# Optimization experiments

Measured on AMD Instinct MI355X. Metric: run time of the kernel, lower is better.

Reference implementation:

```python
import jax, jax.numpy as jnp
import numpy as np


def _conv2d(x, w, b, stride):
    y = jax.lax.conv_general_dilated(x, w, (stride, stride), [(1, 1), (1, 1)],
                                     dimension_numbers=('NCHW', 'OIHW', 'NCHW'))
    return y + b[None, :, None, None]


def _bn(x, g, b, m, v, eps=1e-5):
    scale = g * jax.lax.rsqrt(v + eps)
    return x * scale[None, :, None, None] + (b - m * scale)[None, :, None, None]


def _ln(x, g, b, eps=1e-5):
    mu = x.mean(-1, keepdims=True)
    var = x.var(-1, keepdims=True)
    return (x - mu) * jax.lax.rsqrt(var + eps) * g + b


def _sru_layer(x, W, v, b, lng, lnb):
    # x: (T,B,D); W: (2,D,4d); v,b: (2,2,d). Bidirectional SRU layer with
    # layer-norm on input, tanh activation, k=4 (highway transform of input).
    xn = _ln(x, lng, lnb)
    d = W.shape[-1] // 4
    B = x.shape[1]
    outs = []
    for direc in range(2):
        xi = xn if direc == 0 else xn[::-1]
        U = xi @ W[direc]                       # (T,B,4d)
        xt, fp, rp, xp = jnp.split(U, 4, axis=-1)
        vf, vr = v[direc, 0], v[direc, 1]
        bf, br = b[direc, 0], b[direc, 1]

        def step(c, u):
            xt_, fp_, rp_, xp_ = u
            f = jax.nn.sigmoid(fp_ + vf * c + bf)   # forget gate, peeks c_{t-1}
            r = jax.nn.sigmoid(rp_ + vr * c + br)   # reset/highway gate
            c_new = f * c + (1.0 - f) * xt_
            h = r * jnp.tanh(c_new) + (1.0 - r) * xp_
            return c_new, h

        c0 = jnp.zeros((B, d), x.dtype)
        _, h = jax.lax.scan(step, c0, (xt, fp, rp, xp))
        outs.append(h if direc == 0 else h[::-1])
    return jnp.concatenate(outs, axis=-1)       # (T,B,2d)


def _forward(x, cnn_w, cnn_b, res_c1w, res_c1b, res_bn1g, res_bn1b, res_bn1m,
             res_bn1v, res_c2w, res_c2b, res_bn2g, res_bn2b, res_bn2m, res_bn2v,
             proj_W, sru_W, sru_v, sru_b, sru_lng, sru_lnb,
             cls_lng, cls_lnb, cls_W1, cls_W2):
    y = _conv2d(x, cnn_w, cnn_b, 2)              # (B,32,F/2,T/2)
    for i in range(res_c1w.shape[0]):            # residual CNN blocks
        r = y
        y = jax.nn.relu(_bn(_conv2d(y, res_c1w[i], res_c1b[i], 1),
                            res_bn1g[i], res_bn1b[i], res_bn1m[i], res_bn1v[i]))
        y = _bn(_conv2d(y, res_c2w[i], res_c2b[i], 1),
                res_bn2g[i], res_bn2b[i], res_bn2m[i], res_bn2v[i])
        y = jax.nn.relu(y + r)
    B, C, H, T = y.shape
    y = y.reshape(B, C * H, T).transpose(2, 0, 1)   # (T,B,C*H)
    y = y @ proj_W                                   # proj_input_to_hidden_first
    for l in range(sru_W.shape[0]):
        y = _sru_layer(y, sru_W[l], sru_v[l], sru_b[l], sru_lng[l], sru_lnb[l])
    y = y.transpose(1, 0, 2)                         # (B,T,2*hid)
    y = _ln(y, cls_lng, cls_lnb)
    y = jax.nn.relu(y @ cls_W1)
    return y @ cls_W2                                # (B,T,n_vocab+1)


def setup_inputs() -> dict:
    key = jax.random.key(0)
    ks = iter(jax.random.split(key, 40))
    nk = lambda: next(ks)
    B, T, F, C = 16, 1024, 128, 32
    L_cnn, L_rnn, hid, vocab = 3, 4, 512, 28
    Din = (F // 2) * C          # 2048
    D = 2 * hid                 # 1024 (bidirectional width)
    rnd = lambda shape, s=0.02: jax.random.normal(nk(), shape, jnp.float32) * s
    return {
        'x': jax.random.normal(nk(), (B, 1, F, T), jnp.float32),
        'cnn_w': rnd((C, 1, 3, 3), 0.1), 'cnn_b': jnp.zeros((C,), jnp.float32),
        'res_c1w': rnd((L_cnn, C, C, 3, 3), 0.05), 'res_c1b': jnp.zeros((L_cnn, C), jnp.float32),
        'res_bn1g': jnp.ones((L_cnn, C), jnp.float32), 'res_bn1b': jnp.zeros((L_cnn, C), jnp.float32),
        'res_bn1m': jnp.zeros((L_cnn, C), jnp.float32), 'res_bn1v': jnp.ones((L_cnn, C), jnp.float32),
        'res_c2w': rnd((L_cnn, C, C, 3, 3), 0.05), 'res_c2b': jnp.zeros((L_cnn, C), jnp.float32),
        'res_bn2g': jnp.ones((L_cnn, C), jnp.float32), 'res_bn2b': jnp.zeros((L_cnn, C), jnp.float32),
        'res_bn2m': jnp.zeros((L_cnn, C), jnp.float32), 'res_bn2v': jnp.ones((L_cnn, C), jnp.float32),
        'proj_W': rnd((Din, D)),
        'sru_W': rnd((L_rnn, 2, D, 4 * hid)),
        'sru_v': rnd((L_rnn, 2, 2, hid)),
        'sru_b': jnp.zeros((L_rnn, 2, 2, hid), jnp.float32),
        'sru_lng': jnp.ones((L_rnn, D), jnp.float32), 'sru_lnb': jnp.zeros((L_rnn, D), jnp.float32),
        'cls_lng': jnp.ones((D,), jnp.float32), 'cls_lnb': jnp.zeros((D,), jnp.float32),
        'cls_W1': rnd((D, hid)), 'cls_W2': rnd((hid, vocab + 1)),
    }


def reference(x, cnn_w, cnn_b, res_c1w, res_c1b, res_bn1g, res_bn1b, res_bn1m,
              res_bn1v, res_c2w, res_c2b, res_bn2g, res_bn2b, res_bn2m, res_bn2v,
              proj_W, sru_W, sru_v, sru_b, sru_lng, sru_lnb,
              cls_lng, cls_lnb, cls_W1, cls_W2):
    return _forward(x, cnn_w, cnn_b, res_c1w, res_c1b, res_bn1g, res_bn1b,
                    res_bn1m, res_bn1v, res_c2w, res_c2b, res_bn2g, res_bn2b,
                    res_bn2m, res_bn2v, proj_W, sru_W, sru_v, sru_b,
                    sru_lng, sru_lnb, cls_lng, cls_lnb, cls_W1, cls_W2)
```

## Files before the change

kernel.cpp:

```cpp
#include <hip/hip_runtime.h>
#include <cstddef>

#define DEVFN __device__ __forceinline__

typedef __attribute__((ext_vector_type(8))) short short8;
typedef __attribute__((ext_vector_type(8))) unsigned short ushort8;
typedef __attribute__((ext_vector_type(4))) float f32x4;
typedef __attribute__((ext_vector_type(2))) unsigned int u32x2;

DEVFN float sigmoidf_(float x) { return 1.0f / (1.0f + __expf(-x)); }
DEVFN float tanh_fast(float x) {
    float e = __expf(2.0f * x);
    return 1.0f - 2.0f / (e + 1.0f);
}
DEVFN unsigned short f2bf(float f) {
    unsigned int u = __float_as_uint(f);
    return (unsigned short)((u + 0x7FFFu + ((u >> 16) & 1u)) >> 16);
}
DEVFN float b2f(unsigned int bits) { return __uint_as_float(bits << 16); }

DEVFN void gload_lds16(const ushort* g, ushort* l) {
    __builtin_amdgcn_global_load_lds(
        (const __attribute__((address_space(1))) unsigned int*)g,
        (__attribute__((address_space(3))) unsigned int*)l, 16, 0, 0);
}

#define PADN 17371008u

__global__ __launch_bounds__(256)
void ring_zero(ushort* A, ushort* B)
{
    int idx = blockIdx.x * 256 + threadIdx.x;
    if (idx >= 296960) return;
    size_t uoff;
    if (idx < 263168) {
        int b = idx / 16448, r = idx % 16448;
        int hs = (r < 8224) ? 0 : 65;
        int o = (r < 8224) ? r : r - 8224;
        uoff = (((size_t)(b * 66 + hs) * 514) * 32 + (size_t)o * 2) >> 1;
    } else {
        int j = idx - 263168;
        int b = j / 2112, r = j % 2112;
        int hs = r >> 5, e = r & 31;
        int wsp = (e < 16) ? 0 : 513;
        int c2 = e & 15;
        uoff = (((size_t)(b * 66 + hs) * 514 + wsp) * 32 + (size_t)c2 * 2) >> 1;
    }
    ((uint*)A)[uoff] = 0; ((uint*)B)[uoff] = 0;
}

__global__ __launch_bounds__(256)
void conv_wprep(const float* __restrict__ c1w, const float* __restrict__ c2w,
                ushort* __restrict__ whi, ushort* __restrict__ wlo)
{
    const int lay = blockIdx.x;
    const int i = lay >> 1;
    const float* src = (lay & 1) ? (c2w + i * 9216) : (c1w + i * 9216);
    for (int e = threadIdx.x; e < 9216; e += 256) {
        int co = e / 288, rem = e % 288, ci = rem / 9, q = rem % 9;
        float v = src[e];
        unsigned short hi = f2bf(v);
        unsigned short lo = f2bf(v - b2f(hi));
        int dst = ((lay * 9 + q) * 32 + co) * 32 + ci;
        whi[dst] = hi; wlo[dst] = lo;
    }
}

__global__ __launch_bounds__(256)
void conv_stem_p(const float* __restrict__ x, const float* __restrict__ w,
                 const float* __restrict__ cb, ushort* __restrict__ Xhi)
{
    const int b = blockIdx.z;
    const int h = blockIdx.y * 4 + (threadIdx.x >> 6);
    const int wc = blockIdx.x * 64 + (threadIdx.x & 63);
    float iv[9];
#pragma unroll
    for (int kh = 0; kh < 3; ++kh)
#pragma unroll
        for (int kw = 0; kw < 3; ++kw) {
            int ih = 2 * h - 1 + kh, iw = 2 * wc - 1 + kw;
            iv[kh * 3 + kw] = (ih >= 0 && ih < 128 && iw >= 0 && iw < 1024)
                ? x[(size_t)b * 131072 + (size_t)ih * 1024 + iw] : 0.0f;
        }
    unsigned short hi[32];
#pragma unroll
    for (int co = 0; co < 32; ++co) {
        const float* wp = w + co * 9;
        float a = cb[co];
#pragma unroll
        for (int q = 0; q < 9; ++q) a = fmaf(iv[q], wp[q], a);
        hi[co] = f2bf(a);
    }
    const size_t o = ((size_t)(b * 66 + h + 1) * 514 + wc + 1) * 32;
#pragma unroll
    for (int v = 0; v < 4; ++v) {
        ushort8 uh;
#pragma unroll
        for (int e = 0; e < 8; ++e) uh[e] = hi[v * 8 + e];
        *(ushort8*)(Xhi + o + v * 8) = uh;
    }
}

template <int RES>
__global__ __launch_bounds__(256)
void conv_mfma(const ushort* __restrict__ Phi,
               const ushort* __restrict__ gwhi, const ushort* __restrict__ gwlo,
               const float* __restrict__ g, const float* __restrict__ bbn,
               const float* __restrict__ mn, const float* __restrict__ vn,
               const float* __restrict__ cbv,
               const ushort* __restrict__ Rhi, ushort* __restrict__ Ohi)
{
    __shared__ __align__(16) ushort Wsh[9216], Wsl[9216];
    const int tid = threadIdx.x, lane = tid & 63, wv = tid >> 6;
    const int b = blockIdx.z, h0 = blockIdx.y * 4, w0 = blockIdx.x * 128;

    for (int i = tid; i < 1152; i += 256) {
        ((uint4*)Wsh)[i] = ((const uint4*)gwhi)[i];
        ((uint4*)Wsl)[i] = ((const uint4*)gwlo)[i];
    }
    __syncthreads();

    const int wr = wv * 32;
    const int fr = lane & 15, fk = (lane >> 4) * 8;
    const int lo0 = (wr + fr) * 32 + fk;
    const int lo1 = (wr + 16 + fr) * 32 + fk;

    float sc[2], sh[2];
#pragma unroll
    for (int n = 0; n < 2; ++n) {
        const int co = n * 16 + fr;
        sc[n] = g[co] * rsqrtf(vn[co] + 1e-5f);
        sh[n] = bbn[co] - mn[co] * sc[n] + cbv[co] * sc[n];
    }

    short8 A[3][2][3];
#define LOADROW(SL, PR)                                                        \
    {                                                                          \
        const size_t rb_ = ((size_t)(b * 66 + (PR)) * 514 + w0) * 32;          \
        _Pragma("unroll")                                                      \
        for (int kw_ = 0; kw_ < 3; ++kw_) {                                    \
            A[SL][0][kw_] = *(const short8*)(Phi + rb_ + kw_ * 32 + lo0);      \
            A[SL][1][kw_] = *(const short8*)(Phi + rb_ + kw_ * 32 + lo1);      \
        }                                                                      \
    }

    LOADROW(0, h0);
    LOADROW(1, h0 + 1);

#pragma unroll
    for (int hh = 0; hh < 4; ++hh) {
        LOADROW((hh + 2) % 3, h0 + hh + 2);
        f32x4 acc[2][2];
#pragma unroll
        for (int m = 0; m < 2; ++m)
#pragma unroll
            for (int n = 0; n < 2; ++n) acc[m][n] = (f32x4){0.f, 0.f, 0.f, 0.f};
#pragma unroll
        for (int kh = 0; kh < 3; ++kh) {
            const int sl = (hh + kh) % 3;
#pragma unroll
            for (int kw = 0; kw < 3; ++kw) {
                const int q = kh * 3 + kw;
                short8 ah0 = A[sl][0][kw];
                short8 ah1 = A[sl][1][kw];
                short8 bh0 = *(const short8*)&Wsh[q * 1024 + fr * 32 + fk];
                short8 bh1 = *(const short8*)&Wsh[q * 1024 + (16 + fr) * 32 + fk];
                short8 bl0 = *(const short8*)&Wsl[q * 1024 + fr * 32 + fk];
                short8 bl1 = *(const short8*)&Wsl[q * 1024 + (16 + fr) * 32 + fk];
                acc[0][0] = __builtin_amdgcn_mfma_f32_16x16x32_bf16(ah0, bh0, acc[0][0], 0, 0, 0);
                acc[0][1] = __builtin_amdgcn_mfma_f32_16x16x32_bf16(ah0, bh1, acc[0][1], 0, 0, 0);
                acc[1][0] = __builtin_amdgcn_mfma_f32_16x16x32_bf16(ah1, bh0, acc[1][0], 0, 0, 0);
                acc[1][1] = __builtin_amdgcn_mfma_f32_16x16x32_bf16(ah1, bh1, acc[1][1], 0, 0, 0);
                acc[0][0] = __builtin_amdgcn_mfma_f32_16x16x32_bf16(ah0, bl0, acc[0][0], 0, 0, 0);
                acc[0][1] = __builtin_amdgcn_mfma_f32_16x16x32_bf16(ah0, bl1, acc[0][1], 0, 0, 0);
                acc[1][0] = __builtin_amdgcn_mfma_f32_16x16x32_bf16(ah1, bl0, acc[1][0], 0, 0, 0);
                acc[1][1] = __builtin_amdgcn_mfma_f32_16x16x32_bf16(ah1, bl1, acc[1][1], 0, 0, 0);
            }
        }
#pragma unroll
        for (int m = 0; m < 2; ++m)
#pragma unroll
            for (int r = 0; r < 4; ++r) {
                const int wl = wr + m * 16 + (lane >> 4) * 4 + r;
                const size_t oidx =
                    ((size_t)(b * 66 + h0 + hh + 1) * 514 + w0 + wl + 1) * 32;
#pragma unroll
                for (int n = 0; n < 2; ++n) {
                    const int co = n * 16 + fr;
                    float val = acc[m][n][r] * sc[n] + sh[n];
                    if (RES) val += b2f(Rhi[oidx + co]);
                    val = fmaxf(val, 0.0f);
                    Ohi[oidx + co] = f2bf(val);
                }
            }
    }
#undef LOADROW
}

__global__ __launch_bounds__(256)
void gather_pad(const ushort* __restrict__ Xhi, ushort* __restrict__ xrow)
{
    __shared__ ushort tile[64 * 16 * 32];
    const int b = blockIdx.y, w0 = blockIdx.x * 16;
    for (int k = threadIdx.x; k < 4096; k += 256) {
        int h = k >> 6, rem = k & 63, wl = rem >> 2, c8 = (rem & 3) * 8;
        const ushort* src = Xhi + ((size_t)(b * 66 + h + 1) * 514 + w0 + 1 + wl) * 32 + c8;
        *(ushort8*)&tile[(h * 16 + wl) * 32 + c8] = *(const ushort8*)src;
    }
    __syncthreads();
    for (int k = threadIdx.x; k < 4096; k += 256) {
        int wl = k >> 8, rem = k & 255, c = rem >> 3, h8 = (rem & 7) * 8;
        ushort8 v;
#pragma unroll
        for (int e = 0; e < 8; ++e) v[e] = tile[((h8 + e) * 16 + wl) * 32 + c];
        *(ushort8*)&xrow[((size_t)(w0 + wl) * 16 + b) * 2048 + c * 64 + h8] = v;
    }
}

__global__ __launch_bounds__(256)
void wconv_t(const float* __restrict__ W, ushort* __restrict__ Bt,
             int K, int N, int perm, size_t wstr, size_t btstr)
{
    __shared__ float tile[64][65];
    const float* Wp = W + (size_t)blockIdx.z * wstr;
    ushort* Btp = Bt + (size_t)blockIdx.z * btstr;
    const int k0 = blockIdx.x * 64;
    const int n0 = blockIdx.y * 64;
#pragma unroll
    for (int p = 0; p < 16; ++p) {
        int idx = p * 256 + threadIdx.x;
        int kl = idx >> 6, nl = idx & 63;
        tile[kl][nl] = Wp[(size_t)(k0 + kl) * N + n0 + nl];
    }
    __syncthreads();
#pragma unroll
    for (int p = 0; p < 16; ++p) {
        int idx = p * 256 + threadIdx.x;
        int nl = idx >> 6, kl = idx & 63;
        int n = n0 + nl;
        int row = perm ? ((n & 511) * 4 + (n >> 9)) : n;
        Btp[(size_t)row * K + k0 + kl] = f2bf(tile[kl][nl]);
    }
}

__global__ __launch_bounds__(256)
void layernorm1024_bf(const float* __restrict__ x, const float* __restrict__ g,
                      const float* __restrict__ b, ushort* __restrict__ y)
{
    const size_t row = blockIdx.x;
    const float4 v = ((const float4*)(x + row * 1024))[threadIdx.x];
    float s = v.x + v.y + v.z + v.w;
    float s2 = v.x * v.x + v.y * v.y + v.z * v.z + v.w * v.w;
#pragma unroll
    for (int off = 32; off; off >>= 1) {
        s += __shfl_down(s, off);
        s2 += __shfl_down(s2, off);
    }
    __shared__ float red[2][4];
    int wid = threadIdx.x >> 6, lane = threadIdx.x & 63;
    if (lane == 0) { red[0][wid] = s; red[1][wid] = s2; }
    __syncthreads();
    s = red[0][0] + red[0][1] + red[0][2] + red[0][3];
    s2 = red[1][0] + red[1][1] + red[1][2] + red[1][3];
    float mu = s * (1.0f / 1024.0f);
    float var = s2 * (1.0f / 1024.0f) - mu * mu;
    float rstd = rsqrtf(var + 1e-5f);
    float4 gv = ((const float4*)g)[threadIdx.x];
    float4 bv = ((const float4*)b)[threadIdx.x];
    ushort4 o;
    o.x = f2bf((v.x - mu) * rstd * gv.x + bv.x);
    o.y = f2bf((v.y - mu) * rstd * gv.y + bv.y);
    o.z = f2bf((v.z - mu) * rstd * gv.z + bv.z);
    o.w = f2bf((v.w - mu) * rstd * gv.w + bv.w);
    ((ushort4*)(y + row * 1024))[threadIdx.x] = o;
}

__global__ __launch_bounds__(512, 2)
void gemm256_bf16(const ushort* __restrict__ A, const ushort* __restrict__ Bt,
                  ushort* __restrict__ C, int M, int N, int K)
{
    __shared__ __align__(16) ushort LDS[65536];
    const int tid = threadIdx.x;
    const int lane = tid & 63, w = tid >> 6;
    const int wm = w >> 2, wn = w & 3;
    const int m0 = blockIdx.y * 256, n0 = blockIdx.x * 256;
    const int fr = lane & 15, fk = (lane >> 4) * 8;
    const int NT = K >> 6;

    const int sprow = tid >> 3;
    const int scb0 = (tid & 7) * 16;
    const int wq = w * 512;

    f32x4 acc[8][4];
#pragma unroll
    for (int i = 0; i < 8; ++i)
#pragma unroll
        for (int j = 0; j < 4; ++j) acc[i][j] = (f32x4){0.f, 0.f, 0.f, 0.f};

    auto stage = [&](int dbuf, int isB, int qi, int kt) {
        const int prow = qi * 64 + sprow;
        const int sc = scb0 ^ (((prow >> 2) & 1) << 5);
        const ushort* g = (isB ? (Bt + (size_t)(n0 + prow) * K)
                               : (A + (size_t)(m0 + prow) * K))
                          + (kt << 6) + (sc >> 1);
        gload_lds16(g, LDS + (isB ? 32768 : 0) + dbuf * 16384 + qi * 4096 + wq);
    };
    auto rdA = [&](int dbuf, int mi8, int ks) -> short8 {
        const int row = wm * 128 + mi8 * 16 + fr;
        int e = (row * 64 + ks * 32 + fk) ^ (((row >> 2) & 1) << 4);
        return *(const short8*)&LDS[dbuf * 16384 + e];
    };
    auto rdB = [&](int dbuf, int ni, int ks) -> short8 {
        const int row = wn * 64 + ni * 16 + fr;
        int e = (row * 64 + ks * 32 + fk) ^ (((row >> 2) & 1) << 4);
        return *(const short8*)&LDS[32768 + dbuf * 16384 + e];
    };

#pragma unroll
    for (int qi = 0; qi < 4; ++qi) stage(0, 0, qi, 0);
#pragma unroll
    for (int qi = 0; qi < 4; ++qi) stage(0, 1, qi, 0);

    for (int kt = 0; kt < NT; ++kt) {
        const int cur = kt & 1, nxt = cur ^ 1;
        const bool more = (kt + 1 < NT);
        short8 bfr[4], afr[4];

        if (more) {
            stage(nxt, 0, 0, kt + 1); stage(nxt, 0, 1, kt + 1);
            asm volatile("s_waitcnt vmcnt(2)" ::: "memory");
        } else {
            asm volatile("s_waitcnt vmcnt(0)" ::: "memory");
        }
        __builtin_amdgcn_s_barrier();
#pragma unroll
        for (int ni = 0; ni < 4; ++ni) bfr[ni] = rdB(cur, ni, 0);
#pragma unroll
        for (int mi = 0; mi < 4; ++mi) afr[mi] = rdA(cur, mi, 0);
        __builtin_amdgcn_s_setprio(1);
#pragma unroll
        for (int mi = 0; mi < 4; ++mi)
#pragma unroll
            for (int ni = 0; ni < 4; ++ni)
                acc[mi][ni] = __builtin_amdgcn_mfma_f32_16x16x32_bf16(
                    afr[mi], bfr[ni], acc[mi][ni], 0, 0, 0);
        __builtin_amdgcn_s_setprio(0);

        if (more) { stage(nxt, 0, 2, kt + 1); stage(nxt, 0, 3, kt + 1); }
#pragma unroll
        for (int mi = 0; mi < 4; ++mi) afr[mi] = rdA(cur, 4 + mi, 0);
        __builtin_amdgcn_s_setprio(1);
#pragma unroll
        for (int mi = 0; mi < 4; ++mi)
#pragma unroll
            for (int ni = 0; ni < 4; ++ni)
                acc[4 + mi][ni] = __builtin_amdgcn_mfma_f32_16x16x32_bf16(
                    afr[mi], bfr[ni], acc[4 + mi][ni], 0, 0, 0);
        __builtin_amdgcn_s_setprio(0);

        if (more) { stage(nxt, 1, 0, kt + 1); stage(nxt, 1, 1, kt + 1); }
#pragma unroll
        for (int ni = 0; ni < 4; ++ni) bfr[ni] = rdB(cur, ni, 1);
#pragma unroll
        for (int mi = 0; mi < 4; ++mi) afr[mi] = rdA(cur, mi, 1);
        __builtin_amdgcn_s_setprio(1);
#pragma unroll
        for (int mi = 0; mi < 4; ++mi)
#pragma unroll
            for (int ni = 0; ni < 4; ++ni)
                acc[mi][ni] = __builtin_amdgcn_mfma_f32_16x16x32_bf16(
                    afr[mi], bfr[ni], acc[mi][ni], 0, 0, 0);
        __builtin_amdgcn_s_setprio(0);

        if (more) { stage(nxt, 1, 2, kt + 1); stage(nxt, 1, 3, kt + 1); }
#pragma unroll
        for (int mi = 0; mi < 4; ++mi) afr[mi] = rdA(cur, 4 + mi, 1);
        __builtin_amdgcn_s_setprio(1);
#pragma unroll
        for (int mi = 0; mi < 4; ++mi)
#pragma unroll
            for (int ni = 0; ni < 4; ++ni)
                acc[4 + mi][ni] = __builtin_amdgcn_mfma_f32_16x16x32_bf16(
                    afr[mi], bfr[ni], acc[4 + mi][ni], 0, 0, 0);
        __builtin_amdgcn_s_setprio(0);

        __builtin_amdgcn_s_barrier();
    }

#pragma unroll
    for (int mi8 = 0; mi8 < 8; ++mi8)
#pragma unroll
        for (int r = 0; r < 4; ++r) {
            const int row = wm * 128 + mi8 * 16 + (lane >> 4) * 4 + r;
#pragma unroll
            for (int ni = 0; ni < 4; ++ni)
                LDS[row * 256 + wn * 64 + ni * 16 + fr] = f2bf(acc[mi8][ni][r]);
        }
    __builtin_amdgcn_s_barrier();
    const int frow = tid >> 5, fcb = (tid & 31) * 8;
#pragma unroll
    for (int it = 0; it < 16; ++it) {
        const int row = it * 16 + frow;
        ushort8 vv = *(const ushort8*)&LDS[row * 256 + fcb];
        *(ushort8*)&C[(size_t)(m0 + row) * N + n0 + fcb] = vv;
    }
}

template <int RELU>
__global__ __launch_bounds__(256)
void gemm_bf16(const ushort* __restrict__ A, const ushort* __restrict__ Bt,
               float* __restrict__ C, int M, int N, int K)
{
    __shared__ __align__(16) ushort Sh[4][4096];
    const int tid = threadIdx.x;
    const int lane = tid & 63, w = tid >> 6;
    const int m0 = blockIdx.y * 128, n0 = blockIdx.x * 128;
    const int srow = lane >> 2;
    const int skel = (lane & 3) * 8;
    const int wr = (w >> 1) * 64, wcol = (w & 1) * 64;
    const int fr = lane & 15, fk = (lane >> 4) * 8;

    f32x4 acc[4][4];
#pragma unroll
    for (int m = 0; m < 4; ++m)
#pragma unroll
        for (int n = 0; n < 4; ++n) acc[m][n] = (f32x4){0.f, 0.f, 0.f, 0.f};

#pragma unroll
    for (int q = 0; q < 2; ++q) {
        const int ch = w * 2 + q;
        gload_lds16(A + (size_t)(m0 + ch * 16 + srow) * K + skel, &Sh[0][ch * 512]);
        gload_lds16(Bt + (size_t)(n0 + ch * 16 + srow) * K + skel, &Sh[2][ch * 512]);
    }
    __syncthreads();

    int cur = 0;
    for (int k0 = 0; k0 < K; k0 += 32) {
        if (k0 + 32 < K) {
#pragma unroll
            for (int q = 0; q < 2; ++q) {
                const int ch = w * 2 + q;
                gload_lds16(A + (size_t)(m0 + ch * 16 + srow) * K + k0 + 32 + skel,
                            &Sh[cur ^ 1][ch * 512]);
                gload_lds16(Bt + (size_t)(n0 + ch * 16 + srow) * K + k0 + 32 + skel,
                            &Sh[2 + (cur ^ 1)][ch * 512]);
            }
        }
        short8 a[4], b[4];
#pragma unroll
        for (int m = 0; m < 4; ++m)
            a[m] = *(const short8*)&Sh[cur][(wr + m * 16 + fr) * 32 + fk];
#pragma unroll
        for (int n = 0; n < 4; ++n)
            b[n] = *(const short8*)&Sh[2 + cur][(wcol + n * 16 + fr) * 32 + fk];
#pragma unroll
        for (int m = 0; m < 4; ++m)
#pragma unroll
            for (int n = 0; n < 4; ++n)
                acc[m][n] = __builtin_amdgcn_mfma_f32_16x16x32_bf16(
                    a[m], b[n], acc[m][n], 0, 0, 0);
        __syncthreads();
        cur ^= 1;
    }
#pragma unroll
    for (int m = 0; m < 4; ++m) {
#pragma unroll
        for (int r = 0; r < 4; ++r) {
            const int row = m0 + wr + m * 16 + (lane >> 4) * 4 + r;
            const size_t rb = (size_t)row * N;
#pragma unroll
            for (int n = 0; n < 4; ++n) {
                float val = acc[m][n][r];
                if (RELU) val = fmaxf(val, 0.0f);
                C[rb + n0 + wcol + n * 16 + fr] = val;
            }
        }
    }
}

__global__ __launch_bounds__(64)
void sru_scan2(const ushort* __restrict__ U, const float* __restrict__ v,
               const float* __restrict__ bb, float* __restrict__ out)
{
    const int gidx = blockIdx.x * 64 + threadIdx.x;
    const int dir = gidx >> 13;
    const int idx = gidx & 8191;
    const int j = idx & 511, b = idx >> 9;
    float vf = v[dir * 1024 + j],   vr = v[dir * 1024 + 512 + j];
    float bf_ = bb[dir * 1024 + j], br_ = bb[dir * 1024 + 512 + j];
    const size_t cb = (size_t)dir * 2048 + j * 4;
    const int co = dir * 512 + j;

    asm volatile("" : "+v"(vf), "+v"(vr), "+v"(bf_), "+v"(br_));
    asm volatile("s_waitcnt vmcnt(0)" ::: "memory");

#define TT(q_) (dir ? (511 - (q_)) : (q_))
    float c = 0.0f;
    u32x2 A[16], B[16];

#define ISSUE(dst, s_)                                                         \
    asm volatile("global_load_dwordx2 %0, %1, off"                             \
                 : "=v"(dst)                                                   \
                 : "v"(U + (((size_t)(TT(s_) * 16 + b)) << 12) + cb)           \
                 : "memory")
#define FILL(BUF, wn_)                                                         \
    {                                                                          \
        _Pragma("unroll")                                                      \
        for (int q_ = 0; q_ < 16; ++q_) ISSUE(BUF[q_], (wn_) * 16 + q_);       \
    }
#define WAITBUF(BUF)                                                           \
    asm volatile("s_waitcnt vmcnt(16)"                                         \
                 : "+v"(BUF[0]), "+v"(BUF[1]), "+v"(BUF[2]), "+v"(BUF[3]),     \
                   "+v"(BUF[4]), "+v"(BUF[5]), "+v"(BUF[6]), "+v"(BUF[7]),     \
                   "+v"(BUF[8]), "+v"(BUF[9]), "+v"(BUF[10]), "+v"(BUF[11]),   \
                   "+v"(BUF[12]), "+v"(BUF[13]), "+v"(BUF[14]), "+v"(BUF[15])  \
                 :: "memory")
#define STEP(val, s_)                                                          \
    {                                                                          \
        const int t_ = TT(s_);                                                 \
        float xt = b2f(val[0] & 0xffffu);                                      \
        float fp = b2f(val[0] >> 16);                                          \
        float rp = b2f(val[1] & 0xffffu);                                      \
        float xp = b2f(val[1] >> 16);                                          \
        float f = sigmoidf_(fp + vf * c + bf_);                                \
        float r = sigmoidf_(rp + vr * c + br_);                                \
        c = fmaf(f, c - xt, xt);                                               \
        float h = fmaf(r, tanh_fast(c) - xp, xp);                              \
        asm volatile("global_store_dword %0, %1, off"                          \
                     :: "v"(out + (((size_t)(t_ * 16 + b)) << 10) + co),       \
                        "v"(h)                                                 \
                     : "memory");                                              \
    }

    FILL(A, 0);
    for (int p = 0; p < 16; ++p) {
        const int s0 = p * 32;
        FILL(B, 2 * p + 1);
        WAITBUF(A);
#pragma unroll
        for (int q = 0; q < 16; ++q) STEP(A[q], s0 + q);
        if (p < 15) FILL(A, 2 * p + 2);
        WAITBUF(B);
#pragma unroll
        for (int q = 0; q < 16; ++q) STEP(B[q], s0 + 16 + q);
    }
#undef STEP
#undef WAITBUF
#undef FILL
#undef ISSUE
#undef TT
}

__global__ __launch_bounds__(256)
void cls_out(const float* __restrict__ h1, const float* __restrict__ W2,
             float* __restrict__ out)
{
    const int gidx = blockIdx.x * 256 + threadIdx.x;
    const int n = gidx & 31, m = gidx >> 5;
    if (n >= 29) return;
    const float4* hr = (const float4*)(h1 + (size_t)m * 512);
    float acc = 0.0f;
    for (int k4 = 0; k4 < 128; ++k4) {
        float4 hv = hr[k4];
        const float* wp = W2 + (size_t)(k4 * 4) * 29 + n;
        acc = fmaf(hv.x, wp[0],  acc);
        acc = fmaf(hv.y, wp[29], acc);
        acc = fmaf(hv.z, wp[58], acc);
        acc = fmaf(hv.w, wp[87], acc);
    }
    const int t = m >> 4, b = m & 15;
    out[((size_t)b * 512 + t) * 29 + n] = acc;
}

extern "C" void kernel_launch(void* const* d_in, const int* in_sizes, int n_in,
                              void* d_out, int out_size, void* d_ws, size_t ws_size,
                              hipStream_t stream)
{
    (void)in_sizes; (void)n_in; (void)out_size; (void)ws_size;
    const float* x      = (const float*)d_in[0];
    const float* cnn_w  = (const float*)d_in[1];
    const float* cnn_b  = (const float*)d_in[2];
    const float* c1w    = (const float*)d_in[3];
    const float* c1b    = (const float*)d_in[4];
    const float* bn1g   = (const float*)d_in[5];
    const float* bn1b   = (const float*)d_in[6];
    const float* bn1m   = (const float*)d_in[7];
    const float* bn1v   = (const float*)d_in[8];
    const float* c2w    = (const float*)d_in[9];
    const float* c2b    = (const float*)d_in[10];
    const float* bn2g   = (const float*)d_in[11];
    const float* bn2b   = (const float*)d_in[12];
    const float* bn2m   = (const float*)d_in[13];
    const float* bn2v   = (const float*)d_in[14];
    const float* projW  = (const float*)d_in[15];
    const float* sruW   = (const float*)d_in[16];
    const float* sruV   = (const float*)d_in[17];
    const float* sruB   = (const float*)d_in[18];
    const float* sruLNg = (const float*)d_in[19];
    const float* sruLNb = (const float*)d_in[20];
    const float* clsLNg = (const float*)d_in[21];
    const float* clsLNb = (const float*)d_in[22];
    const float* W1     = (const float*)d_in[23];
    const float* W2     = (const float*)d_in[24];
    float* out = (float*)d_out;
    float* ws  = (float*)d_ws;

    ushort* Xhi = (ushort*)ws;
    ushort* Thi = Xhi + PADN;
    ushort* convw_hi = (ushort*)(ws + 34742016);
    ushort* convw_lo = convw_hi + 55296;
    ushort* xrow_bf  = (ushort*)(ws + 34865152);
    ushort* xn_bf    = (ushort*)(ws + 43253760);
    ushort* Ubuf     = (ushort*)ws;
    float*  xch      = ws + 16777216;
    ushort* proj_bt  = (ushort*)(ws + 25165824);
    ushort* sru_bt   = (ushort*)(ws + 26214400);
    ushort* w1t      = (ushort*)(ws + 34603008);
    float*  h1       = ws;

    dim3 blk(256);

    ring_zero<<<1160, blk, 0, stream>>>(Xhi, Thi);
    conv_wprep<<<6, blk, 0, stream>>>(c1w, c2w, convw_hi, convw_lo);
    conv_stem_p<<<dim3(8, 16, 16), blk, 0, stream>>>(x, cnn_w, cnn_b, Xhi);
    for (int i = 0; i < 3; ++i) {
        const int l1 = 2 * i, l2 = 2 * i + 1;
        conv_mfma<0><<<dim3(4, 16, 16), blk, 0, stream>>>(
            Xhi, convw_hi + l1 * 9216, convw_lo + l1 * 9216,
            bn1g + i * 32, bn1b + i * 32, bn1m + i * 32, bn1v + i * 32,
            c1b + i * 32, nullptr, Thi);
        conv_mfma<1><<<dim3(4, 16, 16), blk, 0, stream>>>(
            Thi, convw_hi + l2 * 9216, convw_lo + l2 * 9216,
            bn2g + i * 32, bn2b + i * 32, bn2m + i * 32, bn2v + i * 32,
            c2b + i * 32, Xhi, Xhi);
    }

    wconv_t<<<dim3(32, 16, 1), blk, 0, stream>>>(projW, proj_bt, 2048, 1024, 0, 0, 0);
    wconv_t<<<dim3(16, 32, 8), blk, 0, stream>>>(sruW, sru_bt, 1024, 2048, 1,
                                                 2097152, 2097152);
    wconv_t<<<dim3(16, 8, 1), blk, 0, stream>>>(W1, w1t, 1024, 512, 0, 0, 0);

    gather_pad<<<dim3(32, 16), blk, 0, stream>>>(Xhi, xrow_bf);

    gemm_bf16<0><<<dim3(8, 64), blk, 0, stream>>>(
        xrow_bf, proj_bt, xch, 8192, 1024, 2048);

    for (int l = 0; l < 4; ++l) {
        layernorm1024_bf<<<8192, blk, 0, stream>>>(
            xch, sruLNg + l * 1024, sruLNb + l * 1024, xn_bf);
        gemm256_bf16<<<dim3(16, 32), dim3(512), 0, stream>>>(
            xn_bf, sru_bt + (size_t)l * 4194304, Ubuf, 8192, 4096, 1024);
        sru_scan2<<<256, dim3(64), 0, stream>>>(
            Ubuf, sruV + l * 2048, sruB + l * 2048, xch);
    }

    layernorm1024_bf<<<8192, blk, 0, stream>>>(xch, clsLNg, clsLNb, xn_bf);
    gemm_bf16<1><<<dim3(4, 64), blk, 0, stream>>>(
        xn_bf, w1t, h1, 8192, 512, 1024);
    cls_out<<<1024, blk, 0, stream>>>(h1, W2, out);
}
```

Measured before the change: 936.1 us.

## Split SRU scan: serial c-chain only, move highway output into fused LN kernel

```diff
diff --git a/kernel.cpp b/kernel.cpp
--- a/kernel.cpp
+++ b/kernel.cpp
@@ -6,7 +6,6 @@
 typedef __attribute__((ext_vector_type(8))) short short8;
 typedef __attribute__((ext_vector_type(8))) unsigned short ushort8;
 typedef __attribute__((ext_vector_type(4))) float f32x4;
-typedef __attribute__((ext_vector_type(2))) unsigned int u32x2;
 
 DEVFN float sigmoidf_(float x) { return 1.0f / (1.0f + __expf(-x)); }
 DEVFN float tanh_fast(float x) {
@@ -275,9 +274,64 @@
     ((ushort4*)(y + row * 1024))[threadIdx.x] = o;
 }
 
+__global__ __launch_bounds__(256)
+void lnh(const float* __restrict__ cbuf, const ushort* __restrict__ Uo,
+         const float* __restrict__ v, const float* __restrict__ bb,
+         const float* __restrict__ g, const float* __restrict__ be,
+         ushort* __restrict__ y)
+{
+    const int r = blockIdx.x, t = r >> 4;
+    const int tid = threadIdx.x, dir = tid >> 7;
+    const int jj = (tid * 4) & 511;
+    float4 cc = *(const float4*)(cbuf + (size_t)r * 1024 + tid * 4);
+    const int pr = dir ? (t == 511 ? -1 : r + 16) : (t == 0 ? -1 : r - 16);
+    float4 cp = {0.f, 0.f, 0.f, 0.f};
+    if (pr >= 0) cp = *(const float4*)(cbuf + (size_t)pr * 1024 + tid * 4);
+    ushort8 u = *(const ushort8*)(Uo + (size_t)r * 2048 + dir * 1024 + jj * 2);
+    float4 vr = *(const float4*)(v + dir * 1024 + 512 + jj);
+    float4 br = *(const float4*)(bb + dir * 1024 + 512 + jj);
+    float h[4];
+    const float cpe[4] = {cp.x, cp.y, cp.z, cp.w};
+    const float cce[4] = {cc.x, cc.y, cc.z, cc.w};
+    const float vre[4] = {vr.x, vr.y, vr.z, vr.w};
+    const float bre[4] = {br.x, br.y, br.z, br.w};
+#pragma unroll
+    for (int e = 0; e < 4; ++e) {
+        float rp = b2f(u[2 * e]);
+        float xp = b2f(u[2 * e + 1]);
+        float rg = sigmoidf_(rp + vre[e] * cpe[e] + bre[e]);
+        h[e] = fmaf(rg, tanh_fast(cce[e]) - xp, xp);
+    }
+    float s = h[0] + h[1] + h[2] + h[3];
+    float s2 = h[0] * h[0] + h[1] * h[1] + h[2] * h[2] + h[3] * h[3];
+#pragma unroll
+    for (int off = 32; off; off >>= 1) {
+        s += __shfl_down(s, off);
+        s2 += __shfl_down(s2, off);
+    }
+    __shared__ float red[2][4];
+    int wid = tid >> 6, lane = tid & 63;
+    if (lane == 0) { red[0][wid] = s; red[1][wid] = s2; }
+    __syncthreads();
+    s = red[0][0] + red[0][1] + red[0][2] + red[0][3];
+    s2 = red[1][0] + red[1][1] + red[1][2] + red[1][3];
+    float mu = s * (1.0f / 1024.0f);
+    float var = s2 * (1.0f / 1024.0f) - mu * mu;
+    float rstd = rsqrtf(var + 1e-5f);
+    float4 gv = ((const float4*)g)[tid];
+    float4 bv = ((const float4*)be)[tid];
+    ushort4 o;
+    o.x = f2bf((h[0] - mu) * rstd * gv.x + bv.x);
+    o.y = f2bf((h[1] - mu) * rstd * gv.y + bv.y);
+    o.z = f2bf((h[2] - mu) * rstd * gv.z + bv.z);
+    o.w = f2bf((h[3] - mu) * rstd * gv.w + bv.w);
+    ((ushort4*)(y + (size_t)r * 1024))[tid] = o;
+}
+
 __global__ __launch_bounds__(512, 2)
 void gemm256_bf16(const ushort* __restrict__ A, const ushort* __restrict__ Bt,
-                  ushort* __restrict__ C, int M, int N, int K)
+                  ushort* __restrict__ Uc, ushort* __restrict__ Uo,
+                  int M, int N, int K)
 {
     __shared__ __align__(16) ushort LDS[65536];
     const int tid = threadIdx.x;
@@ -398,11 +452,21 @@
         }
     __builtin_amdgcn_s_barrier();
     const int frow = tid >> 5, fcb = (tid & 31) * 8;
+    const int g0 = n0 + fcb;
+    const int dirq = g0 >> 11, j0 = (g0 & 2047) >> 2;
+    const size_t cbase = (size_t)dirq * 1024 + j0 * 2;
 #pragma unroll
     for (int it = 0; it < 16; ++it) {
         const int row = it * 16 + frow;
         ushort8 vv = *(const ushort8*)&LDS[row * 256 + fcb];
-        *(ushort8*)&C[(size_t)(m0 + row) * N + n0 + fcb] = vv;
+        uint2 ch, uo;
+        ch.x = (uint)vv[0] | ((uint)vv[1] << 16);
+        ch.y = (uint)vv[4] | ((uint)vv[5] << 16);
+        uo.x = (uint)vv[2] | ((uint)vv[3] << 16);
+        uo.y = (uint)vv[6] | ((uint)vv[7] << 16);
+        const size_t rb = (size_t)(m0 + row) * 2048 + cbase;
+        *(uint2*)&Uc[rb] = ch;
+        *(uint2*)&Uo[rb] = uo;
     }
 }
 
@@ -479,74 +543,79 @@
 }
 
 __global__ __launch_bounds__(64)
-void sru_scan2(const ushort* __restrict__ U, const float* __restrict__ v,
-               const float* __restrict__ bb, float* __restrict__ out)
+void scan_c(const uint* __restrict__ Uc, const float* __restrict__ v,
+            const float* __restrict__ bb, float* __restrict__ cbuf)
 {
     const int gidx = blockIdx.x * 64 + threadIdx.x;
     const int dir = gidx >> 13;
     const int idx = gidx & 8191;
     const int j = idx & 511, b = idx >> 9;
-    float vf = v[dir * 1024 + j],   vr = v[dir * 1024 + 512 + j];
-    float bf_ = bb[dir * 1024 + j], br_ = bb[dir * 1024 + 512 + j];
-    const size_t cb = (size_t)dir * 2048 + j * 4;
-    const int co = dir * 512 + j;
-
-    asm volatile("" : "+v"(vf), "+v"(vr), "+v"(bf_), "+v"(br_));
+    float vf = v[dir * 1024 + j], bf_ = bb[dir * 1024 + j];
+    const int off = b * 1024 + dir * 512 + j;
+    asm volatile("" : "+v"(vf), "+v"(bf_));
     asm volatile("s_waitcnt vmcnt(0)" ::: "memory");
 
 #define TT(q_) (dir ? (511 - (q_)) : (q_))
     float c = 0.0f;
-    u32x2 A[16], B[16];
+    uint A[16], B[16];
 
 #define ISSUE(dst, s_)                                                         \
-    asm volatile("global_load_dwordx2 %0, %1, off"                             \
+    asm volatile("global_load_dword %0, %1, off"                               \
                  : "=v"(dst)                                                   \
-                 : "v"(U + (((size_t)(TT(s_) * 16 + b)) << 12) + cb)           \
+                 : "v"(Uc + ((size_t)TT(s_) * 16384 + off))                    \
                  : "memory")
-#define FILL(BUF, wn_)                                                         \
+#define FILLW(BUF, wn_)                                                        \
     {                                                                          \
         _Pragma("unroll")                                                      \
         for (int q_ = 0; q_ < 16; ++q_) ISSUE(BUF[q_], (wn_) * 16 + q_);       \
     }
-#define WAITBUF(BUF)                                                           \
-    asm volatile("s_waitcnt vmcnt(16)"                                         \
+#define WAITB(BUF, NSTR)                                                       \
+    asm volatile("s_waitcnt vmcnt(" NSTR ")"                                   \
                  : "+v"(BUF[0]), "+v"(BUF[1]), "+v"(BUF[2]), "+v"(BUF[3]),     \
                    "+v"(BUF[4]), "+v"(BUF[5]), "+v"(BUF[6]), "+v"(BUF[7]),     \
                    "+v"(BUF[8]), "+v"(BUF[9]), "+v"(BUF[10]), "+v"(BUF[11]),   \
                    "+v"(BUF[12]), "+v"(BUF[13]), "+v"(BUF[14]), "+v"(BUF[15])  \
                  :: "memory")
-#define STEP(val, s_)                                                          \
+#define STEPC(val, s_)                                                         \
     {                                                                          \
-        const int t_ = TT(s_);                                                 \
-        float xt = b2f(val[0] & 0xffffu);                                      \
-        float fp = b2f(val[0] >> 16);                                          \
-        float rp = b2f(val[1] & 0xffffu);                                      \
-        float xp = b2f(val[1] >> 16);                                          \
+        float xt = b2f(val & 0xffffu);                                         \
+        float fp = b2f(val >> 16);                                             \
         float f = sigmoidf_(fp + vf * c + bf_);                                \
-        float r = sigmoidf_(rp + vr * c + br_);                                \
         c = fmaf(f, c - xt, xt);                                               \
-        float h = fmaf(r, tanh_fast(c) - xp, xp);                              \
         asm volatile("global_store_dword %0, %1, off"                          \
-                     :: "v"(out + (((size_t)(t_ * 16 + b)) << 10) + co),       \
-                        "v"(h)                                                 \
+                     :: "v"(cbuf + ((size_t)TT(s_) * 16384 + off)), "v"(c)     \
                      : "memory");                                              \
     }
 
-    FILL(A, 0);
-    for (int p = 0; p < 16; ++p) {
+    FILLW(A, 0); FILLW(B, 1);
+    WAITB(A, "16");
+#pragma unroll
+    for (int q = 0; q < 16; ++q) STEPC(A[q], q);
+    FILLW(A, 2);
+    WAITB(B, "32");
+#pragma unroll
+    for (int q = 0; q < 16; ++q) STEPC(B[q], 16 + q);
+    FILLW(B, 3);
+    for (int p = 1; p < 15; ++p) {
         const int s0 = p * 32;
-        FILL(B, 2 * p + 1);
-        WAITBUF(A);
-#pragma unroll
-        for (int q = 0; q < 16; ++q) STEP(A[q], s0 + q);
-        if (p < 15) FILL(A, 2 * p + 2);
-        WAITBUF(B);
-#pragma unroll
-        for (int q = 0; q < 16; ++q) STEP(B[q], s0 + 16 + q);
-    }
-#undef STEP
-#undef WAITBUF
-#undef FILL
+        WAITB(A, "32");
+#pragma unroll
+        for (int q = 0; q < 16; ++q) STEPC(A[q], s0 + q);
+        FILLW(A, 2 * p + 2);
+        WAITB(B, "32");
+#pragma unroll
+        for (int q = 0; q < 16; ++q) STEPC(B[q], s0 + 16 + q);
+        FILLW(B, 2 * p + 3);
+    }
+    WAITB(A, "32");
+#pragma unroll
+    for (int q = 0; q < 16; ++q) STEPC(A[q], 480 + q);
+    WAITB(B, "16");
+#pragma unroll
+    for (int q = 0; q < 16; ++q) STEPC(B[q], 496 + q);
+#undef STEPC
+#undef WAITB
+#undef FILLW
 #undef ISSUE
 #undef TT
 }
@@ -611,8 +680,9 @@
     ushort* convw_lo = convw_hi + 55296;
     ushort* xrow_bf  = (ushort*)(ws + 34865152);
     ushort* xn_bf    = (ushort*)(ws + 43253760);
-    ushort* Ubuf     = (ushort*)ws;
-    float*  xch      = ws + 16777216;
+    ushort* Uchain   = (ushort*)ws;
+    ushort* Uout     = Uchain + 16777216;
+    float*  cbuf     = ws + 16777216;
     ushort* proj_bt  = (ushort*)(ws + 25165824);
     ushort* sru_bt   = (ushort*)(ws + 26214400);
     ushort* w1t      = (ushort*)(ws + 34603008);
@@ -643,18 +713,24 @@
     gather_pad<<<dim3(32, 16), blk, 0, stream>>>(Xhi, xrow_bf);
 
     gemm_bf16<0><<<dim3(8, 64), blk, 0, stream>>>(
-        xrow_bf, proj_bt, xch, 8192, 1024, 2048);
+        xrow_bf, proj_bt, cbuf, 8192, 1024, 2048);
 
     for (int l = 0; l < 4; ++l) {
-        layernorm1024_bf<<<8192, blk, 0, stream>>>(
-            xch, sruLNg + l * 1024, sruLNb + l * 1024, xn_bf);
+        if (l == 0)
+            layernorm1024_bf<<<8192, blk, 0, stream>>>(
+                cbuf, sruLNg, sruLNb, xn_bf);
+        else
+            lnh<<<8192, blk, 0, stream>>>(
+                cbuf, Uout, sruV + (l - 1) * 2048, sruB + (l - 1) * 2048,
+                sruLNg + l * 1024, sruLNb + l * 1024, xn_bf);
         gemm256_bf16<<<dim3(16, 32), dim3(512), 0, stream>>>(
-            xn_bf, sru_bt + (size_t)l * 4194304, Ubuf, 8192, 4096, 1024);
-        sru_scan2<<<256, dim3(64), 0, stream>>>(
-            Ubuf, sruV + l * 2048, sruB + l * 2048, xch);
-    }
-
-    layernorm1024_bf<<<8192, blk, 0, stream>>>(xch, clsLNg, clsLNb, xn_bf);
+            xn_bf, sru_bt + (size_t)l * 4194304, Uchain, Uout, 8192, 4096, 1024);
+        scan_c<<<256, dim3(64), 0, stream>>>(
+            (const uint*)Uchain, sruV + l * 2048, sruB + l * 2048, cbuf);
+    }
+
+    lnh<<<8192, blk, 0, stream>>>(
+        cbuf, Uout, sruV + 3 * 2048, sruB + 3 * 2048, clsLNg, clsLNb, xn_bf);
     gemm_bf16<1><<<dim3(4, 64), blk, 0, stream>>>(
         xn_bf, w1t, h1, 8192, 512, 1024);
     cls_out<<<1024, blk, 0, stream>>>(h1, W2, out);
```

Result: faster. 813.1 us (-13.1%).
